# Optimization experiments

Hardware: AMD Instinct MI355X
Metric: run time of the kernel (lower is better)

Reference implementation:

```python
import jax, jax.numpy as jnp
import numpy as np

NUM_CLUSTERS = 32   # matches labels fill_max; clusters_dim after per-batch unique+pad
DELTA_VAR = 1.0
DELTA_DIST = 2.0
VAR_W = 1.0
DIST_W = 1.0
REG_W = 1.0
EPS = 1e-12  # keeps sqrt differentiable at 0 (torch .norm has 0 subgradient there)


def _loss(data, labels):
    B, d, H, W = data.shape
    C = NUM_CLUSTERS
    N = H * W
    x = data.reshape(B, d, N)                                   # [B,d,N]
    ind = jax.nn.one_hot(labels.reshape(B, N), C, dtype=jnp.float32)  # [B,N,C]
    c_sizes = ind.sum(1)                                        # [B,C]
    real = (c_sizes > 0).astype(jnp.float32)
    dummy = 1.0 - real
    n_clusters = real.sum(1)                                    # [B]
    inv_sizes = real / (c_sizes + dummy)                        # 1/size, 0 for empty
    # cluster centers: masked segment-mean
    centers = jnp.einsum('bdn,bnc->bcd', x, ind) * inv_sizes[:, :, None]  # [B,C,d]
    # point-to-center distances via expanded squared-norm (avoids [B,C,N,d])
    x2 = jnp.sum(x * x, axis=1)                                 # [B,N]
    c2 = jnp.sum(centers * centers, axis=2)                     # [B,C]
    dot = jnp.einsum('bcd,bdn->bcn', centers, x)                # [B,C,N]
    d2 = jnp.maximum(x2[:, None, :] + c2[:, :, None] - 2.0 * dot, EPS)
    err = jnp.square(jnp.maximum(jnp.sqrt(d2) - DELTA_VAR, 0.0))  # [B,C,N]
    var_terms = jnp.einsum('bnc,bcn->bc', ind, err) * inv_sizes   # [B,C]
    var_term = jnp.mean(jnp.sum(var_terms, axis=1) / n_clusters)
    # pairwise center distances
    cdot = jnp.einsum('bcd,bed->bce', centers, centers)         # [B,C,C]
    cd2 = jnp.maximum(c2[:, :, None] + c2[:, None, :] - 2.0 * cdot, EPS)
    dist_mat = jnp.sqrt(cd2)
    eye = jnp.eye(C, dtype=jnp.float32)
    masked = dist_mat + DELTA_DIST * (eye[None, :, :] + dummy[:, None, :] + dummy[:, :, None])
    cost = jnp.square(jnp.maximum(DELTA_DIST - masked, 0.0))    # [B,C,C]
    cluster_pairs = n_clusters * (n_clusters - 1.0) / 2.0
    dist_term = jnp.mean(jnp.sum(cost, axis=(1, 2)) / 2.0 / cluster_pairs)
    # regularization on center norms; delta_reg defaults to sqrt(d)
    delta_reg = jnp.float32(np.sqrt(d))
    cnorm = jnp.sqrt(jnp.maximum(c2, EPS))
    reg_term = jnp.mean(jnp.sum(jnp.square(jnp.maximum(cnorm - delta_reg, 0.0)), axis=1) / n_clusters)
    return VAR_W * var_term + DIST_W * dist_term + REG_W * reg_term


def setup_inputs() -> dict:
    key = jax.random.key(0)
    k1, k2 = jax.random.split(key)
    data = jax.random.normal(k1, (8, 64, 256, 256), dtype=jnp.float32)
    labels = jax.random.randint(k2, (8, 256, 256), 0, NUM_CLUSTERS)
    return {"data": data, "labels": labels}


def reference(data, labels):
    return _loss(data, labels)
```

## Files before the change

### kernel.cpp

```cpp
#include <hip/hip_runtime.h>
#include <math.h>

#define NB 8
#define ND 64
#define NN 65536
#define NC 32
#define NSPLIT 2
constexpr float EPSF = 1e-12f;


__global__ __launch_bounds__(256) void k_sums(const float* __restrict__ data,
                                              const int* __restrict__ labels,
                                              float* __restrict__ sums2,
                                              float* __restrict__ countsf) {
    const int d = blockIdx.x, split = blockIdx.y, b = blockIdx.z;
    const int tid = threadIdx.x;
    __shared__ float bins[NC][256];
    for (int i = tid; i < NC * 256 / 4; i += 256)
        ((float4*)bins)[i] = float4{0.f, 0.f, 0.f, 0.f};
    __syncthreads();
    const int Q = NN / NSPLIT / 4;
    const int4* lp = (const int4*)(labels + (size_t)b * NN) + (size_t)split * Q;
    if (d == ND) {
        for (int i = tid; i < Q; i += 1024) {
            int4 c0 = lp[i], c1 = lp[i + 256], c2 = lp[i + 512], c3 = lp[i + 768];
            bins[c0.x & 31][tid] += 1.f; bins[c0.y & 31][tid] += 1.f;
            bins[c0.z & 31][tid] += 1.f; bins[c0.w & 31][tid] += 1.f;
            bins[c1.x & 31][tid] += 1.f; bins[c1.y & 31][tid] += 1.f;
            bins[c1.z & 31][tid] += 1.f; bins[c1.w & 31][tid] += 1.f;
            bins[c2.x & 31][tid] += 1.f; bins[c2.y & 31][tid] += 1.f;
            bins[c2.z & 31][tid] += 1.f; bins[c2.w & 31][tid] += 1.f;
            bins[c3.x & 31][tid] += 1.f; bins[c3.y & 31][tid] += 1.f;
            bins[c3.z & 31][tid] += 1.f; bins[c3.w & 31][tid] += 1.f;
        }
    } else {
        const float4* xp = (const float4*)(data + ((size_t)b * ND + d) * NN) + (size_t)split * Q;
        for (int i = tid; i < Q; i += 1024) {
            float4 x0 = xp[i], x1 = xp[i + 256], x2 = xp[i + 512], x3 = xp[i + 768];
            int4 c0 = lp[i], c1 = lp[i + 256], c2 = lp[i + 512], c3 = lp[i + 768];
            bins[c0.x & 31][tid] += x0.x; bins[c0.y & 31][tid] += x0.y;
            bins[c0.z & 31][tid] += x0.z; bins[c0.w & 31][tid] += x0.w;
            bins[c1.x & 31][tid] += x1.x; bins[c1.y & 31][tid] += x1.y;
            bins[c1.z & 31][tid] += x1.z; bins[c1.w & 31][tid] += x1.w;
            bins[c2.x & 31][tid] += x2.x; bins[c2.y & 31][tid] += x2.y;
            bins[c2.z & 31][tid] += x2.z; bins[c2.w & 31][tid] += x2.w;
            bins[c3.x & 31][tid] += x3.x; bins[c3.y & 31][tid] += x3.y;
            bins[c3.z & 31][tid] += x3.z; bins[c3.w & 31][tid] += x3.w;
        }
    }
    __syncthreads();
    const int c = tid >> 3, j = tid & 7;
    float s = 0.f;
#pragma unroll
    for (int i = 0; i < 32; ++i) s += bins[c][i * 8 + j];
    s += __shfl_xor(s, 1);
    s += __shfl_xor(s, 2);
    s += __shfl_xor(s, 4);
    if (j == 0) {
        if (d == ND) countsf[((size_t)split * NB + b) * NC + c] = s;
        else sums2[(((size_t)split * NB + b) * NC + c) * ND + d] = s;
    }
}

__global__ __launch_bounds__(256) void k_centers(const float* __restrict__ sums2,
                                                 const float* __restrict__ countsf,
                                                 float* __restrict__ centersT2,
                                                 float* __restrict__ c2g,
                                                 float* __restrict__ wg,
                                                 float* __restrict__ cterm) {
    const int b = blockIdx.x, tid = threadIdx.x;
    __shared__ float cent[NC][ND];
    __shared__ float invs[NC], reals[NC], c2s[NC];
    __shared__ float ncl_s;
    __shared__ float red[4];
    if (tid < NC) {
        float cntv = 0.f;
#pragma unroll
        for (int s = 0; s < NSPLIT; ++s) cntv += countsf[((size_t)s * NB + b) * NC + tid];
        reals[tid] = cntv > 0.f ? 1.f : 0.f;
        invs[tid]  = cntv > 0.f ? 1.f / cntv : 0.f;
    }
    __syncthreads();
    if (tid == 0) {
        float nc = 0.f;
        for (int c = 0; c < NC; ++c) nc += reals[c];
        ncl_s = nc;
    }
    for (int i = tid; i < NC * ND; i += 256) {
        int c = i >> 6, d = i & 63;
        float v = 0.f;
#pragma unroll
        for (int s = 0; s < NSPLIT; ++s)
            v += sums2[(((size_t)s * NB + b) * NC + c) * ND + d];
        v *= invs[c];
        cent[c][d] = v;
        centersT2[(size_t)b * 2048 + (size_t)(d >> 1) * 64 + c * 2 + (d & 1)] = v;
    }
    __syncthreads();
    {
        int c = tid >> 3, j = tid & 7;
        float s = 0.f;
#pragma unroll
        for (int i = 0; i < 8; ++i) { float v = cent[c][j * 8 + i]; s = fmaf(v, v, s); }
        s += __shfl_xor(s, 1);
        s += __shfl_xor(s, 2);
        s += __shfl_xor(s, 4);
        if (j == 0) { c2s[c] = s; c2g[b * NC + c] = s; }
    }
    __syncthreads();
    const float ncl = ncl_s;
    if (tid < NC) wg[b * NC + tid] = invs[tid] / (ncl * (float)NB);
    float acc = 0.f;
#pragma unroll
    for (int k = 0; k < 4; ++k) {
        int p = tid * 4 + k;
        int c = p >> 5, e = p & (NC - 1);
        if (c != e && reals[c] > 0.f && reals[e] > 0.f) {
            float cd = 0.f;
            for (int dd = 0; dd < ND; ++dd) cd = fmaf(cent[c][dd], cent[e][dd], cd);
            float cd2 = fmaxf(c2s[c] + c2s[e] - 2.f * cd, EPSF);
            float m = fmaxf(2.f - sqrtf(cd2), 0.f);
            acc += m * m;
        }
    }
    const float pairs = ncl * (ncl - 1.f) * 0.5f;
    acc = acc / (2.f * pairs * (float)NB);
    if (tid < NC) {
        float cn = sqrtf(fmaxf(c2s[tid], EPSF));
        float m = fmaxf(cn - 8.f, 0.f);
        acc += (m * m) / (ncl * (float)NB);
    }
#pragma unroll
    for (int o = 32; o >= 1; o >>= 1) acc += __shfl_xor(acc, o);
    if ((tid & 63) == 0) red[tid >> 6] = acc;
    __syncthreads();
    if (tid == 0) cterm[b] = red[0] + red[1] + red[2] + red[3];
}

__global__ __launch_bounds__(256) void k_var(const float* __restrict__ data,
                                             const int* __restrict__ labels,
                                             const float* __restrict__ centersT2,
                                             const float* __restrict__ c2g,
                                             const float* __restrict__ wg,
                                             float* __restrict__ partials) {
    const int chunk = blockIdx.x, b = blockIdx.y, tid = threadIdx.x;
    __shared__ float2 cT2[32][NC];
    __shared__ float c2s[NC], wsm[NC];
    __shared__ float red[4];
    const int n0 = chunk * 1024 + tid * 4;
    int4 cv = *(const int4*)(labels + (size_t)b * NN + n0);
    for (int i = tid; i < 512; i += 256)
        ((float4*)cT2)[i] = ((const float4*)(centersT2 + (size_t)b * 2048))[i];
    if (tid < NC) { c2s[tid] = c2g[b * NC + tid]; wsm[tid] = wg[b * NC + tid]; }
    __syncthreads();
    const int cx = cv.x & 31, cy = cv.y & 31, cz = cv.z & 31, cw = cv.w & 31;
    const float* base = data + (size_t)b * ND * NN + n0;
    float dp0 = 0, dp1 = 0, dp2 = 0, dp3 = 0, q0 = 0, q1 = 0, q2 = 0, q3 = 0;
#pragma unroll 8
    for (int d2 = 0; d2 < 32; ++d2) {
        float4 xa = *(const float4*)(base + (size_t)(2 * d2) * NN);
        float4 xb = *(const float4*)(base + (size_t)(2 * d2 + 1) * NN);
        float2 ca = cT2[d2][cx], cb = cT2[d2][cy], cc = cT2[d2][cz], cd = cT2[d2][cw];
        dp0 = fmaf(xa.x, ca.x, dp0); dp0 = fmaf(xb.x, ca.y, dp0);
        dp1 = fmaf(xa.y, cb.x, dp1); dp1 = fmaf(xb.y, cb.y, dp1);
        dp2 = fmaf(xa.z, cc.x, dp2); dp2 = fmaf(xb.z, cc.y, dp2);
        dp3 = fmaf(xa.w, cd.x, dp3); dp3 = fmaf(xb.w, cd.y, dp3);
        q0 = fmaf(xa.x, xa.x, q0); q0 = fmaf(xb.x, xb.x, q0);
        q1 = fmaf(xa.y, xa.y, q1); q1 = fmaf(xb.y, xb.y, q1);
        q2 = fmaf(xa.z, xa.z, q2); q2 = fmaf(xb.z, xb.z, q2);
        q3 = fmaf(xa.w, xa.w, q3); q3 = fmaf(xb.w, xb.w, q3);
    }
    float t0 = fmaxf(q0 + c2s[cx] - 2.f * dp0, EPSF);
    float t1 = fmaxf(q1 + c2s[cy] - 2.f * dp1, EPSF);
    float t2 = fmaxf(q2 + c2s[cz] - 2.f * dp2, EPSF);
    float t3 = fmaxf(q3 + c2s[cw] - 2.f * dp3, EPSF);
    float e0 = fmaxf(sqrtf(t0) - 1.f, 0.f);
    float e1 = fmaxf(sqrtf(t1) - 1.f, 0.f);
    float e2 = fmaxf(sqrtf(t2) - 1.f, 0.f);
    float e3 = fmaxf(sqrtf(t3) - 1.f, 0.f);
    float acc = e0 * e0 * wsm[cx] + e1 * e1 * wsm[cy] + e2 * e2 * wsm[cz] + e3 * e3 * wsm[cw];
#pragma unroll
    for (int o = 32; o >= 1; o >>= 1) acc += __shfl_xor(acc, o);
    if ((tid & 63) == 0) red[tid >> 6] = acc;
    __syncthreads();
    if (tid == 0) partials[b * 64 + chunk] = red[0] + red[1] + red[2] + red[3];
}

__global__ __launch_bounds__(256) void k_final(const float* __restrict__ partials,
                                               const float* __restrict__ cterm,
                                               float* __restrict__ out) {
    const int tid = threadIdx.x;
    __shared__ float red[4];
    float s = 0.f;
    for (int i = tid; i < NB * 64; i += 256) s += partials[i];
    if (tid < NB) s += cterm[tid];
#pragma unroll
    for (int o = 32; o >= 1; o >>= 1) s += __shfl_xor(s, o);
    if ((tid & 63) == 0) red[tid >> 6] = s;
    __syncthreads();
    if (tid == 0) out[0] = red[0] + red[1] + red[2] + red[3];
}

extern "C" void kernel_launch(void* const* d_in, const int* in_sizes, int n_in,
                              void* d_out, int out_size, void* d_ws, size_t ws_size,
                              hipStream_t stream) {
    const float* data  = (const float*)d_in[0];
    const int* labels  = (const int*)d_in[1];
    float* out = (float*)d_out;
    float* ws  = (float*)d_ws;
    float* sums2     = ws;
    float* countsf   = ws + 32768;
    float* centersT2 = ws + 33280;
    float* c2g       = ws + 49664;
    float* wg        = ws + 49920;
    float* cterm     = ws + 50176;
    float* partials  = ws + 50184;

    k_sums<<<dim3(ND + 1, NSPLIT, NB), 256, 0, stream>>>(data, labels, sums2, countsf);
    k_centers<<<NB, 256, 0, stream>>>(sums2, countsf, centersT2, c2g, wg, cterm);
    k_var<<<dim3(NN / 1024, NB), 256, 0, stream>>>(data, labels, centersT2, c2g, wg, partials);
    k_final<<<1, 256, 0, stream>>>(partials, cterm, out);
}
```

Measured before the change: 232.7 us.

## Fuse center computation into variance kernel and prefetch loads in sums kernel

Removes the separate centers and final-reduction kernels. Each variance block now recomputes the cluster centers from the partial sums in shared memory, and chunk 0 also computes the distance and regularization terms. Results are accumulated into the output with atomics, and the output is zeroed inside the sums kernel. The sums kernel loop also gains software prefetching of the next iteration's data and labels. This cuts two kernel launches and their serialization, at the cost of redundant center recomputation in every block and nondeterministic float atomic ordering.

After: 221.7 us. 1.05x faster.

```diff
diff --git a/kernel.cpp b/kernel.cpp
--- a/kernel.cpp
+++ b/kernel.cpp
@@ -12,12 +12,14 @@
 __global__ __launch_bounds__(256) void k_sums(const float* __restrict__ data,
                                               const int* __restrict__ labels,
                                               float* __restrict__ sums2,
-                                              float* __restrict__ countsf) {
+                                              float* __restrict__ countsf,
+                                              float* __restrict__ out) {
     const int d = blockIdx.x, split = blockIdx.y, b = blockIdx.z;
     const int tid = threadIdx.x;
     __shared__ float bins[NC][256];
     for (int i = tid; i < NC * 256 / 4; i += 256)
         ((float4*)bins)[i] = float4{0.f, 0.f, 0.f, 0.f};
+    if (d == ND && split == 0 && b == 0 && tid == 0) out[0] = 0.f;
     __syncthreads();
     const int Q = NN / NSPLIT / 4;
     const int4* lp = (const int4*)(labels + (size_t)b * NN) + (size_t)split * Q;
@@ -35,9 +37,17 @@
         }
     } else {
         const float4* xp = (const float4*)(data + ((size_t)b * ND + d) * NN) + (size_t)split * Q;
-        for (int i = tid; i < Q; i += 1024) {
-            float4 x0 = xp[i], x1 = xp[i + 256], x2 = xp[i + 512], x3 = xp[i + 768];
-            int4 c0 = lp[i], c1 = lp[i + 256], c2 = lp[i + 512], c3 = lp[i + 768];
+        float4 x0 = xp[tid], x1 = xp[tid + 256], x2 = xp[tid + 512], x3 = xp[tid + 768];
+        int4  c0 = lp[tid], c1 = lp[tid + 256], c2 = lp[tid + 512], c3 = lp[tid + 768];
+        for (int i = tid;;) {
+            const int nxt = i + 1024;
+            const bool more = (nxt < Q);
+            float4 y0, y1, y2, y3;
+            int4 e0, e1, e2, e3;
+            if (more) {
+                y0 = xp[nxt]; y1 = xp[nxt + 256]; y2 = xp[nxt + 512]; y3 = xp[nxt + 768];
+                e0 = lp[nxt]; e1 = lp[nxt + 256]; e2 = lp[nxt + 512]; e3 = lp[nxt + 768];
+            }
             bins[c0.x & 31][tid] += x0.x; bins[c0.y & 31][tid] += x0.y;
             bins[c0.z & 31][tid] += x0.z; bins[c0.w & 31][tid] += x0.w;
             bins[c1.x & 31][tid] += x1.x; bins[c1.y & 31][tid] += x1.y;
@@ -46,6 +56,10 @@
             bins[c2.z & 31][tid] += x2.z; bins[c2.w & 31][tid] += x2.w;
             bins[c3.x & 31][tid] += x3.x; bins[c3.y & 31][tid] += x3.y;
             bins[c3.z & 31][tid] += x3.z; bins[c3.w & 31][tid] += x3.w;
+            if (!more) break;
+            x0 = y0; x1 = y1; x2 = y2; x3 = y3;
+            c0 = e0; c1 = e1; c2 = e2; c3 = e3;
+            i = nxt;
         }
     }
     __syncthreads();
@@ -62,23 +76,22 @@
     }
 }
 
-__global__ __launch_bounds__(256) void k_centers(const float* __restrict__ sums2,
-                                                 const float* __restrict__ countsf,
-                                                 float* __restrict__ centersT2,
-                                                 float* __restrict__ c2g,
-                                                 float* __restrict__ wg,
-                                                 float* __restrict__ cterm) {
-    const int b = blockIdx.x, tid = threadIdx.x;
-    __shared__ float cent[NC][ND];
-    __shared__ float invs[NC], reals[NC], c2s[NC];
+__global__ __launch_bounds__(256) void k_var(const float* __restrict__ data,
+                                             const int* __restrict__ labels,
+                                             const float* __restrict__ sums2,
+                                             const float* __restrict__ countsf,
+                                             float* __restrict__ out) {
+    const int chunk = blockIdx.x, b = blockIdx.y, tid = threadIdx.x;
+    __shared__ float2 cT2[32][NC];
+    __shared__ float c2s[NC], wsm[NC], invs[NC], reals[NC];
     __shared__ float ncl_s;
-    __shared__ float red[4];
+    __shared__ float red[4], red2[4];
+    const int n0 = chunk * 1024 + tid * 4;
+    int4 cv = *(const int4*)(labels + (size_t)b * NN + n0);
     if (tid < NC) {
-        float cntv = 0.f;
-#pragma unroll
-        for (int s = 0; s < NSPLIT; ++s) cntv += countsf[((size_t)s * NB + b) * NC + tid];
-        reals[tid] = cntv > 0.f ? 1.f : 0.f;
-        invs[tid]  = cntv > 0.f ? 1.f / cntv : 0.f;
+        float cnt = countsf[b * NC + tid] + countsf[(NB + b) * NC + tid];
+        reals[tid] = cnt > 0.f ? 1.f : 0.f;
+        invs[tid]  = cnt > 0.f ? 1.f / cnt : 0.f;
     }
     __syncthreads();
     if (tid == 0) {
@@ -88,71 +101,60 @@
     }
     for (int i = tid; i < NC * ND; i += 256) {
         int c = i >> 6, d = i & 63;
-        float v = 0.f;
-#pragma unroll
-        for (int s = 0; s < NSPLIT; ++s)
-            v += sums2[(((size_t)s * NB + b) * NC + c) * ND + d];
-        v *= invs[c];
-        cent[c][d] = v;
-        centersT2[(size_t)b * 2048 + (size_t)(d >> 1) * 64 + c * 2 + (d & 1)] = v;
+        float v = (sums2[((size_t)b * NC + c) * ND + d] +
+                   sums2[((size_t)(NB + b) * NC + c) * ND + d]) * invs[c];
+        ((float*)cT2)[(d >> 1) * 64 + c * 2 + (d & 1)] = v;
     }
     __syncthreads();
     {
         int c = tid >> 3, j = tid & 7;
         float s = 0.f;
 #pragma unroll
-        for (int i = 0; i < 8; ++i) { float v = cent[c][j * 8 + i]; s = fmaf(v, v, s); }
+        for (int i = 0; i < 8; ++i) {
+            int d = j * 8 + i;
+            float v = ((float*)cT2)[(d >> 1) * 64 + c * 2 + (d & 1)];
+            s = fmaf(v, v, s);
+        }
         s += __shfl_xor(s, 1);
         s += __shfl_xor(s, 2);
         s += __shfl_xor(s, 4);
-        if (j == 0) { c2s[c] = s; c2g[b * NC + c] = s; }
+        if (j == 0) c2s[c] = s;
     }
     __syncthreads();
     const float ncl = ncl_s;
-    if (tid < NC) wg[b * NC + tid] = invs[tid] / (ncl * (float)NB);
-    float acc = 0.f;
-#pragma unroll
-    for (int k = 0; k < 4; ++k) {
-        int p = tid * 4 + k;
-        int c = p >> 5, e = p & (NC - 1);
-        if (c != e && reals[c] > 0.f && reals[e] > 0.f) {
-            float cd = 0.f;
-            for (int dd = 0; dd < ND; ++dd) cd = fmaf(cent[c][dd], cent[e][dd], cd);
-            float cd2 = fmaxf(c2s[c] + c2s[e] - 2.f * cd, EPSF);
-            float m = fmaxf(2.f - sqrtf(cd2), 0.f);
-            acc += m * m;
-        }
-    }
-    const float pairs = ncl * (ncl - 1.f) * 0.5f;
-    acc = acc / (2.f * pairs * (float)NB);
-    if (tid < NC) {
-        float cn = sqrtf(fmaxf(c2s[tid], EPSF));
-        float m = fmaxf(cn - 8.f, 0.f);
-        acc += (m * m) / (ncl * (float)NB);
-    }
-#pragma unroll
-    for (int o = 32; o >= 1; o >>= 1) acc += __shfl_xor(acc, o);
-    if ((tid & 63) == 0) red[tid >> 6] = acc;
-    __syncthreads();
-    if (tid == 0) cterm[b] = red[0] + red[1] + red[2] + red[3];
-}
-
-__global__ __launch_bounds__(256) void k_var(const float* __restrict__ data,
-                                             const int* __restrict__ labels,
-                                             const float* __restrict__ centersT2,
-                                             const float* __restrict__ c2g,
-                                             const float* __restrict__ wg,
-                                             float* __restrict__ partials) {
-    const int chunk = blockIdx.x, b = blockIdx.y, tid = threadIdx.x;
-    __shared__ float2 cT2[32][NC];
-    __shared__ float c2s[NC], wsm[NC];
-    __shared__ float red[4];
-    const int n0 = chunk * 1024 + tid * 4;
-    int4 cv = *(const int4*)(labels + (size_t)b * NN + n0);
-    for (int i = tid; i < 512; i += 256)
-        ((float4*)cT2)[i] = ((const float4*)(centersT2 + (size_t)b * 2048))[i];
-    if (tid < NC) { c2s[tid] = c2g[b * NC + tid]; wsm[tid] = wg[b * NC + tid]; }
-    __syncthreads();
+    if (tid < NC) wsm[tid] = invs[tid] / (ncl * (float)NB);
+    __syncthreads();
+    if (chunk == 0) {
+        float acc = 0.f;
+#pragma unroll
+        for (int k = 0; k < 4; ++k) {
+            int p = tid * 4 + k;
+            int c = p >> 5, e = p & (NC - 1);
+            if (c != e && reals[c] > 0.f && reals[e] > 0.f) {
+                float cd = 0.f;
+                for (int d2 = 0; d2 < 32; ++d2) {
+                    float2 a = cT2[d2][c], bb = cT2[d2][e];
+                    cd = fmaf(a.x, bb.x, cd);
+                    cd = fmaf(a.y, bb.y, cd);
+                }
+                float cd2 = fmaxf(c2s[c] + c2s[e] - 2.f * cd, EPSF);
+                float m = fmaxf(2.f - sqrtf(cd2), 0.f);
+                acc += m * m;
+            }
+        }
+        const float pairs = ncl * (ncl - 1.f) * 0.5f;
+        acc = acc / (2.f * pairs * (float)NB);
+        if (tid < NC) {
+            float cn = sqrtf(fmaxf(c2s[tid], EPSF));
+            float m = fmaxf(cn - 8.f, 0.f);
+            acc += (m * m) / (ncl * (float)NB);
+        }
+#pragma unroll
+        for (int o = 32; o >= 1; o >>= 1) acc += __shfl_xor(acc, o);
+        if ((tid & 63) == 0) red[tid >> 6] = acc;
+        __syncthreads();
+        if (tid == 0) unsafeAtomicAdd(out, red[0] + red[1] + red[2] + red[3]);
+    }
     const int cx = cv.x & 31, cy = cv.y & 31, cz = cv.z & 31, cw = cv.w & 31;
     const float* base = data + (size_t)b * ND * NN + n0;
     float dp0 = 0, dp1 = 0, dp2 = 0, dp3 = 0, q0 = 0, q1 = 0, q2 = 0, q3 = 0;
@@ -181,24 +183,9 @@
     float acc = e0 * e0 * wsm[cx] + e1 * e1 * wsm[cy] + e2 * e2 * wsm[cz] + e3 * e3 * wsm[cw];
 #pragma unroll
     for (int o = 32; o >= 1; o >>= 1) acc += __shfl_xor(acc, o);
-    if ((tid & 63) == 0) red[tid >> 6] = acc;
-    __syncthreads();
-    if (tid == 0) partials[b * 64 + chunk] = red[0] + red[1] + red[2] + red[3];
-}
-
-__global__ __launch_bounds__(256) void k_final(const float* __restrict__ partials,
-                                               const float* __restrict__ cterm,
-                                               float* __restrict__ out) {
-    const int tid = threadIdx.x;
-    __shared__ float red[4];
-    float s = 0.f;
-    for (int i = tid; i < NB * 64; i += 256) s += partials[i];
-    if (tid < NB) s += cterm[tid];
-#pragma unroll
-    for (int o = 32; o >= 1; o >>= 1) s += __shfl_xor(s, o);
-    if ((tid & 63) == 0) red[tid >> 6] = s;
-    __syncthreads();
-    if (tid == 0) out[0] = red[0] + red[1] + red[2] + red[3];
+    if ((tid & 63) == 0) red2[tid >> 6] = acc;
+    __syncthreads();
+    if (tid == 0) unsafeAtomicAdd(out, red2[0] + red2[1] + red2[2] + red2[3]);
 }
 
 extern "C" void kernel_launch(void* const* d_in, const int* in_sizes, int n_in,
@@ -208,16 +195,9 @@
     const int* labels  = (const int*)d_in[1];
     float* out = (float*)d_out;
     float* ws  = (float*)d_ws;
-    float* sums2     = ws;
-    float* countsf   = ws + 32768;
-    float* centersT2 = ws + 33280;
-    float* c2g       = ws + 49664;
-    float* wg        = ws + 49920;
-    float* cterm     = ws + 50176;
-    float* partials  = ws + 50184;
-
-    k_sums<<<dim3(ND + 1, NSPLIT, NB), 256, 0, stream>>>(data, labels, sums2, countsf);
-    k_centers<<<NB, 256, 0, stream>>>(sums2, countsf, centersT2, c2g, wg, cterm);
-    k_var<<<dim3(NN / 1024, NB), 256, 0, stream>>>(data, labels, centersT2, c2g, wg, partials);
-    k_final<<<1, 256, 0, stream>>>(partials, cterm, out);
+    float* sums2   = ws;
+    float* countsf = ws + 32768;
+
+    k_sums<<<dim3(ND + 1, NSPLIT, NB), 256, 0, stream>>>(data, labels, sums2, countsf, out);
+    k_var<<<dim3(NN / 1024, NB), 256, 0, stream>>>(data, labels, sums2, countsf, out);
 }
```
